# Kernel tuning notes

Measured on AMD Instinct MI355X. Metric: run time of the kernel, lower is better.

## Reference

```python
import jax, jax.numpy as jnp
import numpy as np

N = 50000      # num nodes
E = 800000     # num edges (before self loops)
B = 50         # num graphs in batch
F_IN = 15
C = 64         # hidden_channels
H = 4          # num_heads
NEG_SLOPE = 0.2  # PyG GATConv default


def setup_inputs() -> dict:
    key = jax.random.key(0)
    ks = jax.random.split(key, 32)
    s = 0.05
    inp = {
        "x": jax.random.normal(ks[0], (N, F_IN), dtype=jnp.float32),
        "edge_index": jax.random.randint(ks[1], (2, E), 0, N, dtype=jnp.int32),
        "batch": jnp.sort(jax.random.randint(ks[2], (N,), 0, B, dtype=jnp.int32)),
        "W1": jax.random.normal(ks[3], (F_IN, H * C)) * s,
        "aS1": jax.random.normal(ks[4], (H, C)) * s,
        "aD1": jax.random.normal(ks[5], (H, C)) * s,
        "b1": jnp.zeros((H * C,)),
        "W2": jax.random.normal(ks[6], (H * C, H * C)) * s,
        "aS2": jax.random.normal(ks[7], (H, C)) * s,
        "aD2": jax.random.normal(ks[8], (H, C)) * s,
        "b2": jnp.zeros((H * C,)),
        # GAT layer 3: 256 -> 64, 1 head
        "W3": jax.random.normal(ks[9], (H * C, C)) * s,
        "aS3": jax.random.normal(ks[10], (1, C)) * s,
        "aD3": jax.random.normal(ks[11], (1, C)) * s,
        "b3": jnp.zeros((C,)),
        # node attention MLP: 64 -> 32 -> 1
        "Wna1": jax.random.normal(ks[12], (C, 32)) * s,
        "bna1": jnp.zeros((32,)),
        "Wna2": jax.random.normal(ks[13], (32, 1)) * s,
        "bna2": jnp.zeros((1,)),
        # graph classifier: 128 -> 128 -> 64 -> 1
        "Wc1": jax.random.normal(ks[14], (2 * C, 128)) * s,
        "bc1": jnp.zeros((128,)),
        "Wc2": jax.random.normal(ks[15], (128, 64)) * s,
        "bc2": jnp.zeros((64,)),
        "Wc3": jax.random.normal(ks[16], (64, 1)) * s,
        "bc3": jnp.zeros((1,)),
    }
    return inp


def _gat_conv(x, src, dst, W, a_src, a_dst, b, heads, ch):
    """PyG-style GATConv (add_self_loops=True, negative_slope=0.2, eval mode)."""
    n = x.shape[0]
    h = (x @ W).reshape(n, heads, ch)               # [N, H, C]
    alpha_s = jnp.einsum('nhc,hc->nh', h, a_src)    # per-node src score
    alpha_d = jnp.einsum('nhc,hc->nh', h, a_dst)
    loops = jnp.arange(n, dtype=src.dtype)
    s = jnp.concatenate([src, loops])               # [E+N]
    d = jnp.concatenate([dst, loops])
    e = jax.nn.leaky_relu(alpha_s[s] + alpha_d[d], NEG_SLOPE)   # [E+N, H]
    # segment softmax over incoming edges of each dst node
    m = jax.ops.segment_max(e, d, num_segments=n)
    ex = jnp.exp(e - m[d])
    denom = jax.ops.segment_sum(ex, d, num_segments=n)
    alpha = ex / denom[d]                           # [E+N, H]
    msg = h[s] * alpha[:, :, None]                  # [E+N, H, C]
    out = jax.ops.segment_sum(msg, d, num_segments=n)  # [N, H, C]
    return out.reshape(n, heads * ch) + b


def reference(x, edge_index, batch, W1, aS1, aD1, b1, W2, aS2, aD2, b2,
              W3, aS3, aD3, b3, Wna1, bna1, Wna2, bna2,
              Wc1, bc1, Wc2, bc2, Wc3, bc3):
    src, dst = edge_index[0], edge_index[1]
    x1 = jax.nn.elu(_gat_conv(x, src, dst, W1, aS1, aD1, b1, H, C))
    x2 = jax.nn.elu(_gat_conv(x1, src, dst, W2, aS2, aD2, b2, H, C))
    x3 = jax.nn.elu(_gat_conv(x2, src, dst, W3, aS3, aD3, b3, 1, C))  # [N, 64]

    # node attention: MLP then softmax over ALL nodes (dim=0, as in source)
    na = jax.nn.relu(x3 @ Wna1 + bna1) @ Wna2 + bna2   # [N, 1]
    node_attention = jax.nn.softmax(na, axis=0)

    # graph pooling
    ones = jnp.ones((x3.shape[0],), dtype=x3.dtype)
    cnt = jax.ops.segment_sum(ones, batch, num_segments=B)         # [B]
    mean = jax.ops.segment_sum(x3, batch, num_segments=B) / jnp.maximum(cnt, 1.0)[:, None]
    mx = jax.ops.segment_max(x3, batch, num_segments=B)
    mx = jnp.where(cnt[:, None] > 0, mx, 0.0)
    g = jnp.concatenate([mean, mx], axis=1)                        # [B, 128]

    h1 = jax.nn.relu(g @ Wc1 + bc1)
    h2 = jax.nn.relu(h1 @ Wc2 + bc2)
    risk = jax.nn.sigmoid(h2 @ Wc3 + bc3)                          # [B, 1]
    return (risk, node_attention)
```

## Files before the change

kernel.cpp:

```cpp
#include <hip/hip_runtime.h>
#include <math.h>

#define NN 50000
#define NP 50176
#define EE 800000
#define ETOT (EE + NN)
#define BB 50
#define PC 16

typedef unsigned short u16;
typedef unsigned char u8;
typedef __attribute__((ext_vector_type(8))) short short8;
typedef __attribute__((ext_vector_type(4))) float floatx4;
typedef __attribute__((ext_vector_type(2))) float floatx2;

__device__ __forceinline__ float b2f(u16 u) {
  return __int_as_float(((int)u) << 16);
}
__device__ __forceinline__ u16 f2b(float f) {
  unsigned u = __float_as_uint(f);
  unsigned r = (u + 0x7fffu + ((u >> 16) & 1u)) >> 16;
  return (u16)r;
}
__device__ __forceinline__ u8 f2f8(float v) {
  return (u8)(__builtin_amdgcn_cvt_pk_fp8_f32(v, v, 0, false) & 0xFF);
}
__device__ __forceinline__ float readlane_f(float v, int l) {
  return __int_as_float(__builtin_amdgcn_readlane(__float_as_int(v), l));
}
__device__ __forceinline__ float blo(unsigned w) { return __uint_as_float(w << 16); }
__device__ __forceinline__ float bhi(unsigned w) { return __uint_as_float(w & 0xffff0000u); }

__global__ void count_kernel(const int* __restrict__ ei, int* __restrict__ cnt) {
  int e = blockIdx.x * blockDim.x + threadIdx.x;
  if (e >= ETOT) return;
  int d = (e < EE) ? ei[EE + e] : (e - EE);
  atomicAdd(&cnt[d], 1);
}

__global__ void scan1_kernel(const int* __restrict__ cnt, int* __restrict__ rowp,
                             int* __restrict__ part) {
  __shared__ int s[512];
  int t = threadIdx.x;
  int i = blockIdx.x * 512 + t;
  int v = (i < NN) ? cnt[i] : 0;
  s[t] = v;
  __syncthreads();
  for (int off = 1; off < 512; off <<= 1) {
    int add = (t >= off) ? s[t - off] : 0;
    __syncthreads();
    s[t] += add;
    __syncthreads();
  }
  if (i < NN) rowp[i] = s[t] - v;
  if (t == 511) part[blockIdx.x] = s[511];
}

__global__ void scan2_kernel(int* __restrict__ part, int* __restrict__ rowp) {
  __shared__ int s[128];
  int t = threadIdx.x;
  int v = (t < 98) ? part[t] : 0;
  s[t] = v;
  __syncthreads();
  for (int off = 1; off < 128; off <<= 1) {
    int add = (t >= off) ? s[t - off] : 0;
    __syncthreads();
    s[t] += add;
    __syncthreads();
  }
  if (t < 98) part[t] = s[t] - v;
  if (t == 97) rowp[NN] = s[97];
}

__global__ void scan3_kernel(int* __restrict__ rowp, const int* __restrict__ part) {
  int i = blockIdx.x * 512 + threadIdx.x;
  if (i < NN) rowp[i] += part[blockIdx.x];
}

__global__ void fill_kernel(const int* __restrict__ ei, const int* __restrict__ rowp,
                            int* __restrict__ cur, int* __restrict__ col) {
  int e = blockIdx.x * blockDim.x + threadIdx.x;
  if (e >= ETOT) return;
  int s, d;
  if (e < EE) { s = ei[e]; d = ei[EE + e]; } else { s = e - EE; d = s; }
  int p = atomicAdd(&cur[d], 1);
  col[rowp[d] + p] = s;
}

__global__ void prep_kernel(const float* __restrict__ x, const float* __restrict__ W1,
                            const float* __restrict__ W2, const float* __restrict__ W3,
                            u16* __restrict__ xb, u16* __restrict__ W1t,
                            u16* __restrict__ W2t, u16* __restrict__ W3t) {
  const int T0 = NP * 32, T1 = T0 + 8192, T2 = T1 + 65536, T3 = T2 + 16384;
  int i = blockIdx.x * 256 + threadIdx.x;
  if (i < T0) {
    int n = i >> 5, c = i & 31;
    xb[i] = (n < NN && c < 15) ? f2b(x[n * 15 + c]) : (u16)0;
  } else if (i < T1) {
    int j = i - T0, n = j >> 5, k = j & 31;
    W1t[j] = (k < 15) ? f2b(W1[k * 256 + n]) : (u16)0;
  } else if (i < T2) {
    int j = i - T1, n = j >> 8, k = j & 255;
    W2t[j] = f2b(W2[k * 256 + n]);
  } else if (i < T3) {
    int j = i - T2, n = j >> 8, k = j & 255;
    W3t[j] = f2b(W3[k * 64 + n]);
  }
}

template <int BK, bool F8>
__global__ __launch_bounds__(256) void gemm_bf16_kernel(
    const u16* __restrict__ A, const u16* __restrict__ Bt, u16* __restrict__ C,
    u8* __restrict__ C8, int K, int N, const float* __restrict__ aS,
    const float* __restrict__ aD, float* __restrict__ as_o,
    float* __restrict__ ad_o, int Hh) {
  __shared__ u16 Al[128][BK + 8];
  __shared__ u16 Bl[64][BK + 8];
  __shared__ float sS[4][64], sD[4][64];
  int R0 = blockIdx.x * 128, C0 = blockIdx.y * 64;
  int wid = threadIdx.x >> 6, lane = threadIdx.x & 63;
  int wr = (wid >> 1) * 64, wc = (wid & 1) * 32;
  int lrow = lane & 15, lk8 = (lane >> 4) * 8;
  int rq = (lane >> 4) * 4;
  const int Q4 = BK / 4;
  const int nA = 128 * Q4, nB = 64 * Q4;
  floatx4 acc[4][2];
#pragma unroll
  for (int i = 0; i < 4; ++i)
#pragma unroll
    for (int j = 0; j < 2; ++j) acc[i][j] = (floatx4){0.f, 0.f, 0.f, 0.f};

  for (int k0 = 0; k0 < K; k0 += BK) {
    for (int c = threadIdx.x; c < nA + nB; c += 256) {
      if (c < nA) {
        int r = c / Q4, o = (c % Q4) * 4;
        *(ushort4*)&Al[r][o] = *(const ushort4*)&A[(size_t)(R0 + r) * K + k0 + o];
      } else {
        int c2 = c - nA;
        int r = c2 / Q4, o = (c2 % Q4) * 4;
        *(ushort4*)&Bl[r][o] = *(const ushort4*)&Bt[(size_t)(C0 + r) * K + k0 + o];
      }
    }
    __syncthreads();
#pragma unroll
    for (int ks = 0; ks < BK / 32; ++ks) {
      short8 a[4], b[2];
#pragma unroll
      for (int i = 0; i < 4; ++i) a[i] = *(const short8*)&Al[wr + i * 16 + lrow][ks * 32 + lk8];
#pragma unroll
      for (int j = 0; j < 2; ++j) b[j] = *(const short8*)&Bl[wc + j * 16 + lrow][ks * 32 + lk8];
#pragma unroll
      for (int i = 0; i < 4; ++i)
#pragma unroll
        for (int j = 0; j < 2; ++j)
          acc[i][j] = __builtin_amdgcn_mfma_f32_16x16x32_bf16(a[i], b[j], acc[i][j], 0, 0, 0);
    }
    __syncthreads();
  }
#pragma unroll
  for (int i = 0; i < 4; ++i)
#pragma unroll
    for (int j = 0; j < 2; ++j)
#pragma unroll
      for (int q = 0; q < 4; ++q) {
        int gr = R0 + wr + i * 16 + rq + q;
        int gc = C0 + wc + j * 16 + lrow;
        if constexpr (F8)
          C8[(size_t)gr * N + gc] = f2f8(acc[i][j][q]);
        else
          C[(size_t)gr * N + gc] = f2b(acc[i][j][q]);
      }
  int hb = blockIdx.y * 64;
  float wS0 = aS[hb + wc + lrow], wS1 = aS[hb + wc + 16 + lrow];
  float wD0 = aD[hb + wc + lrow], wD1 = aD[hb + wc + 16 + lrow];
#pragma unroll
  for (int i = 0; i < 4; ++i)
#pragma unroll
    for (int q = 0; q < 4; ++q) {
      float vS = acc[i][0][q] * wS0 + acc[i][1][q] * wS1;
      float vD = acc[i][0][q] * wD0 + acc[i][1][q] * wD1;
#pragma unroll
      for (int o = 8; o; o >>= 1) {
        vS += __shfl_xor(vS, o, 64);
        vD += __shfl_xor(vD, o, 64);
      }
      if (lrow == 0) {
        int rl = i * 16 + rq + q;
        sS[wid][rl] = vS;
        sD[wid][rl] = vD;
      }
    }
  __syncthreads();
  if (threadIdx.x < 128) {
    int p = threadIdx.x >> 6, r = threadIdx.x & 63;
    int gr = R0 + p * 64 + r;
    as_o[(size_t)gr * Hh + blockIdx.y] = sS[2 * p][r] + sS[2 * p + 1][r];
    ad_o[(size_t)gr * Hh + blockIdx.y] = sD[2 * p][r] + sD[2 * p + 1][r];
  }
}

__global__ __launch_bounds__(256) void agg4_kernel(
    const u8* __restrict__ h8, const float* __restrict__ as_i,
    const float* __restrict__ ad_i, const int* __restrict__ rowp,
    const int* __restrict__ col, const float* __restrict__ bias,
    u16* __restrict__ xo) {
  __shared__ float exs[4][64][4];
  int wid = threadIdx.x >> 6, lane = threadIdx.x & 63;
  int d = blockIdx.x * 4 + wid;
  int rp0 = rowp[d], deg = rowp[d + 1] - rp0;
  float4 add = *(const float4*)&ad_i[(size_t)d * 4];
  int hj = lane >> 4;
  int lq = lane << 2;
  float acc0 = 0.f, acc1 = 0.f, acc2 = 0.f, acc3 = 0.f;
  float den0 = 0.f, den1 = 0.f, den2 = 0.f, den3 = 0.f;

  for (int base = 0; base < deg; base += 64) {
    int i = base + lane;
    bool valid = i < deg;
    int s = valid ? col[rp0 + i] : 0;
    float4 asv = *(const float4*)&as_i[(size_t)s * 4];
    float e0 = asv.x + add.x, e1 = asv.y + add.y, e2 = asv.z + add.z, e3 = asv.w + add.w;
    e0 = (e0 > 0.f) ? e0 : 0.2f * e0;
    e1 = (e1 > 0.f) ? e1 : 0.2f * e1;
    e2 = (e2 > 0.f) ? e2 : 0.2f * e2;
    e3 = (e3 > 0.f) ? e3 : 0.2f * e3;
    float x0 = valid ? __expf(e0) : 0.f;
    float x1 = valid ? __expf(e1) : 0.f;
    float x2 = valid ? __expf(e2) : 0.f;
    float x3 = valid ? __expf(e3) : 0.f;
    den0 += x0; den1 += x1; den2 += x2; den3 += x3;
    *(float4*)&exs[wid][lane][0] = make_float4(x0, x1, x2, x3);
    __threadfence_block();
    int cnt = min(64, deg - base);
    int k8 = cnt & ~7;
    for (int k = 0; k < k8; k += 8) {
      unsigned wv[8];
      float qv[8];
#pragma unroll
      for (int u = 0; u < 8; ++u) {
        int sk = __builtin_amdgcn_readlane(s, k + u);
        qv[u] = exs[wid][k + u][hj];
        wv[u] = *(const unsigned*)&h8[(size_t)sk * 256 + lq];
      }
#pragma unroll
      for (int u = 0; u < 8; ++u) {
        floatx2 lo = __builtin_amdgcn_cvt_pk_f32_fp8(wv[u], false);
        floatx2 hi = __builtin_amdgcn_cvt_pk_f32_fp8(wv[u], true);
        acc0 += qv[u] * lo.x;
        acc1 += qv[u] * lo.y;
        acc2 += qv[u] * hi.x;
        acc3 += qv[u] * hi.y;
      }
    }
    for (int k = k8; k < cnt; ++k) {
      int sk = __builtin_amdgcn_readlane(s, k);
      float qk = exs[wid][k][hj];
      unsigned wv = *(const unsigned*)&h8[(size_t)sk * 256 + lq];
      floatx2 lo = __builtin_amdgcn_cvt_pk_f32_fp8(wv, false);
      floatx2 hi = __builtin_amdgcn_cvt_pk_f32_fp8(wv, true);
      acc0 += qk * lo.x;
      acc1 += qk * lo.y;
      acc2 += qk * hi.x;
      acc3 += qk * hi.y;
    }
  }
#pragma unroll
  for (int o = 32; o; o >>= 1) {
    den0 += __shfl_xor(den0, o, 64);
    den1 += __shfl_xor(den1, o, 64);
    den2 += __shfl_xor(den2, o, 64);
    den3 += __shfl_xor(den3, o, 64);
  }
  float den = (hj == 0) ? den0 : (hj == 1) ? den1 : (hj == 2) ? den2 : den3;
  float inv = 1.f / den;
  float4 bv = *(const float4*)&bias[lq];
  float v0 = acc0 * inv + bv.x;
  float v1 = acc1 * inv + bv.y;
  float v2 = acc2 * inv + bv.z;
  float v3 = acc3 * inv + bv.w;
  v0 = (v0 > 0.f) ? v0 : expm1f(v0);
  v1 = (v1 > 0.f) ? v1 : expm1f(v1);
  v2 = (v2 > 0.f) ? v2 : expm1f(v2);
  v3 = (v3 > 0.f) ? v3 : expm1f(v3);
  ushort4 o4;
  o4.x = f2b(v0); o4.y = f2b(v1); o4.z = f2b(v2); o4.w = f2b(v3);
  ((ushort4*)xo)[(size_t)d * 64 + lane] = o4;
}

__global__ __launch_bounds__(256) void agg1_kernel(
    const u16* __restrict__ h, const float* __restrict__ as_i,
    const float* __restrict__ ad_i, const int* __restrict__ rowp,
    const int* __restrict__ col, const float* __restrict__ bias,
    float* __restrict__ xo) {
  int wid = threadIdx.x >> 6, lane = threadIdx.x & 63;
  int d = blockIdx.x * 4 + wid;
  int rp0 = rowp[d], deg = rowp[d + 1] - rp0;
  float add = ad_i[d];
  float acc = 0.f, den = 0.f;
  for (int base = 0; base < deg; base += 64) {
    int i = base + lane;
    bool valid = i < deg;
    int s = valid ? col[rp0 + i] : 0;
    float e = as_i[s] + add;
    e = (e > 0.f) ? e : 0.2f * e;
    float ex = valid ? __expf(e) : 0.f;
    den += ex;
    int cnt = min(64, deg - base);
    int k8 = cnt & ~7;
    for (int k = 0; k < k8; k += 8) {
      int sA[8];
      float qA[8], hv[8];
#pragma unroll
      for (int u = 0; u < 8; ++u) {
        sA[u] = __builtin_amdgcn_readlane(s, k + u);
        qA[u] = readlane_f(ex, k + u);
      }
#pragma unroll
      for (int u = 0; u < 8; ++u) hv[u] = b2f(h[(size_t)sA[u] * 64 + lane]);
      float p0 = qA[0] * hv[0] + qA[1] * hv[1];
      float p1 = qA[2] * hv[2] + qA[3] * hv[3];
      float p2 = qA[4] * hv[4] + qA[5] * hv[5];
      float p3 = qA[6] * hv[6] + qA[7] * hv[7];
      acc += (p0 + p1) + (p2 + p3);
    }
    for (int k = k8; k < cnt; ++k) {
      int sk = __builtin_amdgcn_readlane(s, k);
      float qk = readlane_f(ex, k);
      acc += qk * b2f(h[(size_t)sk * 64 + lane]);
    }
  }
#pragma unroll
  for (int o = 32; o; o >>= 1) den += __shfl_xor(den, o, 64);
  float v = acc / den + bias[lane];
  v = (v > 0.f) ? v : expm1f(v);
  xo[(size_t)d * 64 + lane] = v;
}

__global__ void na_kernel(const float* __restrict__ x3, const float* __restrict__ W1,
                          const float* __restrict__ b1, const float* __restrict__ W2,
                          const float* __restrict__ b2, float* __restrict__ na,
                          float* __restrict__ gsum) {
  __shared__ float Ws[64 * 32];
  __shared__ float W2s[32];
  __shared__ float sred[4];
  for (int i = threadIdx.x; i < 2048; i += blockDim.x) Ws[i] = W1[i];
  if (threadIdx.x < 32) W2s[threadIdx.x] = W2[threadIdx.x];
  __syncthreads();
  int n = blockIdx.x * blockDim.x + threadIdx.x;
  float ez = 0.f;
  if (n < NN) {
    float hid[32];
#pragma unroll
    for (int j = 0; j < 32; ++j) hid[j] = b1[j];
    const float4* x4 = (const float4*)&x3[(size_t)n * 64];
    for (int kk = 0; kk < 16; ++kk) {
      float4 xv = x4[kk];
#pragma unroll
      for (int j = 0; j < 32; ++j) {
        hid[j] += xv.x * Ws[(kk * 4 + 0) * 32 + j];
        hid[j] += xv.y * Ws[(kk * 4 + 1) * 32 + j];
        hid[j] += xv.z * Ws[(kk * 4 + 2) * 32 + j];
        hid[j] += xv.w * Ws[(kk * 4 + 3) * 32 + j];
      }
    }
    float z = b2[0];
#pragma unroll
    for (int j = 0; j < 32; ++j) z += fmaxf(hid[j], 0.f) * W2s[j];
    ez = __expf(z);
    na[n] = ez;
  }
  float acc = ez;
  for (int o = 32; o; o >>= 1) acc += __shfl_xor(acc, o, 64);
  int wid = threadIdx.x >> 6, lane = threadIdx.x & 63;
  if (lane == 0) sred[wid] = acc;
  __syncthreads();
  if (threadIdx.x == 0) atomicAdd(gsum, sred[0] + sred[1] + sred[2] + sred[3]);
}

__global__ void na_write_kernel(const float* __restrict__ na, const float* __restrict__ gsum,
                                float* __restrict__ out) {
  int n = blockIdx.x * blockDim.x + threadIdx.x;
  if (n >= NN) return;
  out[n] = na[n] / gsum[0];
}

__global__ void pool1_kernel(const float* __restrict__ x3, const int* __restrict__ batch,
                             float* __restrict__ ppsum, float* __restrict__ ppmax) {
  int b = blockIdx.x, c = blockIdx.y;
  int lane = threadIdx.x & 63, wid = threadIdx.x >> 6;
  int lo = 0, hi = NN;
  while (lo < hi) { int m = (lo + hi) >> 1; if (batch[m] < b) lo = m + 1; else hi = m; }
  int start = lo;
  lo = start; hi = NN;
  while (lo < hi) { int m = (lo + hi) >> 1; if (batch[m] < b + 1) lo = m + 1; else hi = m; }
  int end = lo;
  int len = end - start;
  int c0 = start + (int)((long)len * c / PC);
  int c1 = start + (int)((long)len * (c + 1) / PC);
  float acc = 0.f, mx = -INFINITY;
  for (int n = c0 + wid; n < c1; n += 4) {
    float v = x3[(size_t)n * 64 + lane];
    acc += v;
    mx = fmaxf(mx, v);
  }
  __shared__ float ssum[4][64], smax[4][64];
  ssum[wid][lane] = acc;
  smax[wid][lane] = mx;
  __syncthreads();
  if (wid == 0) {
    acc = ssum[0][lane] + ssum[1][lane] + ssum[2][lane] + ssum[3][lane];
    mx = fmaxf(fmaxf(smax[0][lane], smax[1][lane]), fmaxf(smax[2][lane], smax[3][lane]));
    size_t o = ((size_t)c * BB + b) * 64 + lane;
    ppsum[o] = acc;
    ppmax[o] = mx;
  }
}

__global__ void pool2cls_kernel(const float* __restrict__ ppsum, const float* __restrict__ ppmax,
                                const int* __restrict__ batch, const float* __restrict__ Wc1,
                                const float* __restrict__ bc1, const float* __restrict__ Wc2,
                                const float* __restrict__ bc2, const float* __restrict__ Wc3,
                                const float* __restrict__ bc3, float* __restrict__ out) {
  __shared__ float g[128], h1[128], h2[64], scnt;
  int b = blockIdx.x, t = threadIdx.x;
  if (t == 0) {
    int lo = 0, hi = NN;
    while (lo < hi) { int m = (lo + hi) >> 1; if (batch[m] < b) lo = m + 1; else hi = m; }
    int start = lo;
    lo = start; hi = NN;
    while (lo < hi) { int m = (lo + hi) >> 1; if (batch[m] < b + 1) lo = m + 1; else hi = m; }
    scnt = (float)(lo - start);
  }
  float s = 0.f, m = -INFINITY;
  if (t < 64) {
#pragma unroll
    for (int c = 0; c < PC; ++c) {
      size_t o = ((size_t)c * BB + b) * 64 + t;
      s += ppsum[o];
      m = fmaxf(m, ppmax[o]);
    }
  }
  __syncthreads();
  float cnt = scnt;
  if (t < 64) {
    g[t] = (cnt > 0.f) ? s / fmaxf(cnt, 1.f) : 0.f;
    g[64 + t] = (cnt > 0.f) ? m : 0.f;
  }
  __syncthreads();
  float v = bc1[t];
  for (int k = 0; k < 128; ++k) v += g[k] * Wc1[k * 128 + t];
  h1[t] = fmaxf(v, 0.f);
  __syncthreads();
  if (t < 64) {
    float v2 = bc2[t];
    for (int k = 0; k < 128; ++k) v2 += h1[k] * Wc2[k * 64 + t];
    h2[t] = fmaxf(v2, 0.f);
  }
  __syncthreads();
  if (t == 0) {
    float z = bc3[0];
    for (int k = 0; k < 64; ++k) z += h2[k] * Wc3[k];
    out[b] = 1.f / (1.f + expf(-z));
  }
}

extern "C" void kernel_launch(void* const* d_in, const int* in_sizes, int n_in,
                              void* d_out, int out_size, void* d_ws, size_t ws_size,
                              hipStream_t stream) {
  const float* x    = (const float*)d_in[0];
  const int*   ei   = (const int*)d_in[1];
  const int*   batch= (const int*)d_in[2];
  const float* W1 = (const float*)d_in[3];
  const float* aS1= (const float*)d_in[4];
  const float* aD1= (const float*)d_in[5];
  const float* b1 = (const float*)d_in[6];
  const float* W2 = (const float*)d_in[7];
  const float* aS2= (const float*)d_in[8];
  const float* aD2= (const float*)d_in[9];
  const float* b2 = (const float*)d_in[10];
  const float* W3 = (const float*)d_in[11];
  const float* aS3= (const float*)d_in[12];
  const float* aD3= (const float*)d_in[13];
  const float* b3 = (const float*)d_in[14];
  const float* Wna1=(const float*)d_in[15];
  const float* bna1=(const float*)d_in[16];
  const float* Wna2=(const float*)d_in[17];
  const float* bna2=(const float*)d_in[18];
  const float* Wc1=(const float*)d_in[19];
  const float* bc1=(const float*)d_in[20];
  const float* Wc2=(const float*)d_in[21];
  const float* bc2=(const float*)d_in[22];
  const float* Wc3=(const float*)d_in[23];
  const float* bc3=(const float*)d_in[24];
  float* out = (float*)d_out;

  char* w = (char*)d_ws;
  size_t off = 0;
  auto alloc = [&](size_t bytes) {
    void* p = w + off;
    off = (off + bytes + 255) & ~(size_t)255;
    return p;
  };
  u16* xb   = (u16*)alloc((size_t)NP * 32 * 2);
  u16* bufA = (u16*)alloc((size_t)NP * 256 * 2);
  u16* bufB = (u16*)alloc((size_t)NP * 256 * 2);
  u8*  h8   = (u8*)alloc((size_t)NP * 256);
  u16* W1t  = (u16*)alloc((size_t)256 * 32 * 2);
  u16* W2t  = (u16*)alloc((size_t)256 * 256 * 2);
  u16* W3t  = (u16*)alloc((size_t)64 * 256 * 2);
  float* asb  = (float*)alloc((size_t)NP * 4 * 4);
  float* adb  = (float*)alloc((size_t)NP * 4 * 4);
  float* nab  = (float*)alloc((size_t)NN * 4);
  int* rowp = (int*)alloc((size_t)(NN + 1) * 4);
  int* cntb = (int*)alloc((size_t)NN * 4);
  int* curb = (int*)alloc((size_t)NN * 4);
  float* gsum = (float*)alloc(256);
  size_t zspan = (size_t)((char*)gsum + 256 - (char*)cntb);
  int* colb = (int*)alloc((size_t)ETOT * 4);
  int* part = (int*)alloc(128 * 4);
  float* ppsum = (float*)alloc((size_t)PC * BB * 64 * 4);
  float* ppmax = (float*)alloc((size_t)PC * BB * 64 * 4);
  float* x3 = (float*)bufB;
  (void)ws_size; (void)in_sizes; (void)n_in; (void)out_size;

  hipMemsetAsync(cntb, 0, zspan, stream);

  count_kernel<<<(ETOT + 255) / 256, 256, 0, stream>>>(ei, cntb);
  scan1_kernel<<<98, 512, 0, stream>>>(cntb, rowp, part);
  scan2_kernel<<<1, 128, 0, stream>>>(part, rowp);
  scan3_kernel<<<98, 512, 0, stream>>>(rowp, part);
  fill_kernel<<<(ETOT + 255) / 256, 256, 0, stream>>>(ei, rowp, curb, colb);

  const int PREP_TOT = NP * 32 + 8192 + 65536 + 16384;
  prep_kernel<<<(PREP_TOT + 255) / 256, 256, 0, stream>>>(x, W1, W2, W3, xb, W1t, W2t, W3t);

  const int GX = NP / 128;
  gemm_bf16_kernel<32, true><<<dim3(GX, 4), 256, 0, stream>>>(
      xb, W1t, nullptr, h8, 32, 256, aS1, aD1, asb, adb, 4);
  agg4_kernel<<<12500, 256, 0, stream>>>(h8, asb, adb, rowp, colb, b1, bufB);
  gemm_bf16_kernel<64, true><<<dim3(GX, 4), 256, 0, stream>>>(
      bufB, W2t, nullptr, h8, 256, 256, aS2, aD2, asb, adb, 4);
  agg4_kernel<<<12500, 256, 0, stream>>>(h8, asb, adb, rowp, colb, b2, bufB);
  gemm_bf16_kernel<64, false><<<dim3(GX, 1), 256, 0, stream>>>(
      bufB, W3t, bufA, nullptr, 256, 64, aS3, aD3, asb, adb, 1);
  agg1_kernel<<<12500, 256, 0, stream>>>(bufA, asb, adb, rowp, colb, b3, x3);

  na_kernel<<<(NN + 255) / 256, 256, 0, stream>>>(x3, Wna1, bna1, Wna2, bna2, nab, gsum);
  na_write_kernel<<<(NN + 255) / 256, 256, 0, stream>>>(nab, gsum, out + BB);

  pool1_kernel<<<dim3(BB, PC), 256, 0, stream>>>(x3, batch, ppsum, ppmax);
  pool2cls_kernel<<<BB, 128, 0, stream>>>(ppsum, ppmax, batch, Wc1, bc1, Wc2, bc2,
                                          Wc3, bc3, out);
}
```

Baseline: 375.0 us.

## Fuse node-attention MLP into final aggregation and batch agg4 gathers by 16

The node-attention MLP (64->32->1 plus exp) now runs inside the final GAT aggregation kernel, one wave per node, using the freshly computed row held in shared memory. This avoids re-reading x3 in a separate kernel, and a small grid-stride kernel now does the global sum. The agg4 inner loop is also rewritten as a templated 16-wide batch with clamped tail handling, which puts more gathers in flight but makes padded lanes issue redundant loads. The fused kernel now stages 8KB of weights into shared memory in every one of its 12500 blocks, which adds global and LDS traffic.

```diff
diff --git a/kernel.cpp b/kernel.cpp
--- a/kernel.cpp
+++ b/kernel.cpp
@@ -28,8 +28,6 @@
 __device__ __forceinline__ float readlane_f(float v, int l) {
   return __int_as_float(__builtin_amdgcn_readlane(__float_as_int(v), l));
 }
-__device__ __forceinline__ float blo(unsigned w) { return __uint_as_float(w << 16); }
-__device__ __forceinline__ float bhi(unsigned w) { return __uint_as_float(w & 0xffff0000u); }
 
 __global__ void count_kernel(const int* __restrict__ ei, int* __restrict__ cnt) {
   int e = blockIdx.x * blockDim.x + threadIdx.x;
@@ -199,6 +197,31 @@
   }
 }
 
+template <int B>
+__device__ __forceinline__ void agg4_batch(
+    const u8* __restrict__ h8, int s, int kbase, int cnt, int hj, int lq,
+    const float (*__restrict__ exsw)[4], float& a0, float& a1, float& a2, float& a3) {
+  unsigned wv[B];
+  float qv[B];
+#pragma unroll
+  for (int u = 0; u < B; ++u) {
+    int ke = kbase + u;
+    int kc = (ke < cnt) ? ke : (cnt - 1);
+    int sk = __builtin_amdgcn_readlane(s, kc);
+    qv[u] = (ke < cnt) ? exsw[kc][hj] : 0.f;
+    wv[u] = *(const unsigned*)&h8[(size_t)sk * 256 + lq];
+  }
+#pragma unroll
+  for (int u = 0; u < B; ++u) {
+    floatx2 lo = __builtin_amdgcn_cvt_pk_f32_fp8(wv[u], false);
+    floatx2 hi = __builtin_amdgcn_cvt_pk_f32_fp8(wv[u], true);
+    a0 += qv[u] * lo.x;
+    a1 += qv[u] * lo.y;
+    a2 += qv[u] * hi.x;
+    a3 += qv[u] * hi.y;
+  }
+}
+
 __global__ __launch_bounds__(256) void agg4_kernel(
     const u8* __restrict__ h8, const float* __restrict__ as_i,
     const float* __restrict__ ad_i, const int* __restrict__ rowp,
@@ -211,7 +234,8 @@
   float4 add = *(const float4*)&ad_i[(size_t)d * 4];
   int hj = lane >> 4;
   int lq = lane << 2;
-  float acc0 = 0.f, acc1 = 0.f, acc2 = 0.f, acc3 = 0.f;
+  const float(*exsw)[4] = exs[wid];
+  float a0 = 0.f, a1 = 0.f, a2 = 0.f, a3 = 0.f;
   float den0 = 0.f, den1 = 0.f, den2 = 0.f, den3 = 0.f;
 
   for (int base = 0; base < deg; base += 64) {
@@ -232,37 +256,8 @@
     *(float4*)&exs[wid][lane][0] = make_float4(x0, x1, x2, x3);
     __threadfence_block();
     int cnt = min(64, deg - base);
-    int k8 = cnt & ~7;
-    for (int k = 0; k < k8; k += 8) {
-      unsigned wv[8];
-      float qv[8];
-#pragma unroll
-      for (int u = 0; u < 8; ++u) {
-        int sk = __builtin_amdgcn_readlane(s, k + u);
-        qv[u] = exs[wid][k + u][hj];
-        wv[u] = *(const unsigned*)&h8[(size_t)sk * 256 + lq];
-      }
-#pragma unroll
-      for (int u = 0; u < 8; ++u) {
-        floatx2 lo = __builtin_amdgcn_cvt_pk_f32_fp8(wv[u], false);
-        floatx2 hi = __builtin_amdgcn_cvt_pk_f32_fp8(wv[u], true);
-        acc0 += qv[u] * lo.x;
-        acc1 += qv[u] * lo.y;
-        acc2 += qv[u] * hi.x;
-        acc3 += qv[u] * hi.y;
-      }
-    }
-    for (int k = k8; k < cnt; ++k) {
-      int sk = __builtin_amdgcn_readlane(s, k);
-      float qk = exs[wid][k][hj];
-      unsigned wv = *(const unsigned*)&h8[(size_t)sk * 256 + lq];
-      floatx2 lo = __builtin_amdgcn_cvt_pk_f32_fp8(wv, false);
-      floatx2 hi = __builtin_amdgcn_cvt_pk_f32_fp8(wv, true);
-      acc0 += qk * lo.x;
-      acc1 += qk * lo.y;
-      acc2 += qk * hi.x;
-      acc3 += qk * hi.y;
-    }
+    for (int kb = 0; kb < cnt; kb += 16)
+      agg4_batch<16>(h8, s, kb, cnt, hj, lq, exsw, a0, a1, a2, a3);
   }
 #pragma unroll
   for (int o = 32; o; o >>= 1) {
@@ -274,10 +269,10 @@
   float den = (hj == 0) ? den0 : (hj == 1) ? den1 : (hj == 2) ? den2 : den3;
   float inv = 1.f / den;
   float4 bv = *(const float4*)&bias[lq];
-  float v0 = acc0 * inv + bv.x;
-  float v1 = acc1 * inv + bv.y;
-  float v2 = acc2 * inv + bv.z;
-  float v3 = acc3 * inv + bv.w;
+  float v0 = a0 * inv + bv.x;
+  float v1 = a1 * inv + bv.y;
+  float v2 = a2 * inv + bv.z;
+  float v3 = a3 * inv + bv.w;
   v0 = (v0 > 0.f) ? v0 : expm1f(v0);
   v1 = (v1 > 0.f) ? v1 : expm1f(v1);
   v2 = (v2 > 0.f) ? v2 : expm1f(v2);
@@ -287,11 +282,19 @@
   ((ushort4*)xo)[(size_t)d * 64 + lane] = o4;
 }
 
-__global__ __launch_bounds__(256) void agg1_kernel(
+__global__ __launch_bounds__(256) void agg1na_kernel(
     const u16* __restrict__ h, const float* __restrict__ as_i,
     const float* __restrict__ ad_i, const int* __restrict__ rowp,
     const int* __restrict__ col, const float* __restrict__ bias,
-    float* __restrict__ xo) {
+    float* __restrict__ xo, const float* __restrict__ Wna1,
+    const float* __restrict__ bna1, const float* __restrict__ Wna2,
+    const float* __restrict__ bna2, float* __restrict__ na) {
+  __shared__ float Ws[2048];
+  __shared__ float W2s[32];
+  __shared__ float xrow[4][64];
+  for (int i = threadIdx.x; i < 2048; i += 256) Ws[i] = Wna1[i];
+  if (threadIdx.x < 32) W2s[threadIdx.x] = Wna2[threadIdx.x];
+  __syncthreads();
   int wid = threadIdx.x >> 6, lane = threadIdx.x & 63;
   int d = blockIdx.x * 4 + wid;
   int rp0 = rowp[d], deg = rowp[d + 1] - rp0;
@@ -334,47 +337,31 @@
   float v = acc / den + bias[lane];
   v = (v > 0.f) ? v : expm1f(v);
   xo[(size_t)d * 64 + lane] = v;
-}
-
-__global__ void na_kernel(const float* __restrict__ x3, const float* __restrict__ W1,
-                          const float* __restrict__ b1, const float* __restrict__ W2,
-                          const float* __restrict__ b2, float* __restrict__ na,
-                          float* __restrict__ gsum) {
-  __shared__ float Ws[64 * 32];
-  __shared__ float W2s[32];
-  __shared__ float sred[4];
-  for (int i = threadIdx.x; i < 2048; i += blockDim.x) Ws[i] = W1[i];
-  if (threadIdx.x < 32) W2s[threadIdx.x] = W2[threadIdx.x];
-  __syncthreads();
-  int n = blockIdx.x * blockDim.x + threadIdx.x;
-  float ez = 0.f;
-  if (n < NN) {
-    float hid[32];
-#pragma unroll
-    for (int j = 0; j < 32; ++j) hid[j] = b1[j];
-    const float4* x4 = (const float4*)&x3[(size_t)n * 64];
-    for (int kk = 0; kk < 16; ++kk) {
-      float4 xv = x4[kk];
-#pragma unroll
-      for (int j = 0; j < 32; ++j) {
-        hid[j] += xv.x * Ws[(kk * 4 + 0) * 32 + j];
-        hid[j] += xv.y * Ws[(kk * 4 + 1) * 32 + j];
-        hid[j] += xv.z * Ws[(kk * 4 + 2) * 32 + j];
-        hid[j] += xv.w * Ws[(kk * 4 + 3) * 32 + j];
-      }
-    }
-    float z = b2[0];
-#pragma unroll
-    for (int j = 0; j < 32; ++j) z += fmaxf(hid[j], 0.f) * W2s[j];
-    ez = __expf(z);
-    na[n] = ez;
-  }
-  float acc = ez;
+  xrow[wid][lane] = v;
+  __threadfence_block();
+  int j = lane & 31;
+  int coff = (lane >> 5) * 32;
+  float hj = 0.f;
+#pragma unroll
+  for (int c = 0; c < 32; ++c) hj += xrow[wid][coff + c] * Ws[(coff + c) * 32 + j];
+  hj += __shfl_xor(hj, 32, 64);
+  hj += bna1[j];
+  float r = fmaxf(hj, 0.f) * W2s[j];
+#pragma unroll
+  for (int o = 16; o; o >>= 1) r += __shfl_xor(r, o, 64);
+  if (lane == 0) na[d] = __expf(r + bna2[0]);
+}
+
+__global__ void na_sum_kernel(const float* __restrict__ na, float* __restrict__ gsum) {
+  __shared__ float s[4];
+  float acc = 0.f;
+  for (int i = blockIdx.x * blockDim.x + threadIdx.x; i < NN; i += gridDim.x * blockDim.x)
+    acc += na[i];
   for (int o = 32; o; o >>= 1) acc += __shfl_xor(acc, o, 64);
   int wid = threadIdx.x >> 6, lane = threadIdx.x & 63;
-  if (lane == 0) sred[wid] = acc;
-  __syncthreads();
-  if (threadIdx.x == 0) atomicAdd(gsum, sred[0] + sred[1] + sred[2] + sred[3]);
+  if (lane == 0) s[wid] = acc;
+  __syncthreads();
+  if (threadIdx.x == 0) atomicAdd(gsum, s[0] + s[1] + s[2] + s[3]);
 }
 
 __global__ void na_write_kernel(const float* __restrict__ na, const float* __restrict__ gsum,
@@ -543,11 +530,11 @@
   agg4_kernel<<<12500, 256, 0, stream>>>(h8, asb, adb, rowp, colb, b2, bufB);
   gemm_bf16_kernel<64, false><<<dim3(GX, 1), 256, 0, stream>>>(
       bufB, W3t, bufA, nullptr, 256, 64, aS3, aD3, asb, adb, 1);
-  agg1_kernel<<<12500, 256, 0, stream>>>(bufA, asb, adb, rowp, colb, b3, x3);
-
-  na_kernel<<<(NN + 255) / 256, 256, 0, stream>>>(x3, Wna1, bna1, Wna2, bna2, nab, gsum);
+  agg1na_kernel<<<12500, 256, 0, stream>>>(bufA, asb, adb, rowp, colb, b3, x3,
+                                           Wna1, bna1, Wna2, bna2, nab);
+
+  na_sum_kernel<<<196, 256, 0, stream>>>(nab, gsum);
   na_write_kernel<<<(NN + 255) / 256, 256, 0, stream>>>(nab, gsum, out + BB);
-
   pool1_kernel<<<dim3(BB, PC), 256, 0, stream>>>(x3, batch, ppsum, ppmax);
   pool2cls_kernel<<<BB, 128, 0, stream>>>(ppsum, ppmax, batch, Wc1, bc1, Wc2, bc2,
                                           Wc3, bc3, out);
```

Result: slower. 387.1 us (+3.2%).
